# Performance work log

Hardware: AMD Instinct MI355X
Metric: run time of the kernel (lower is better)

The kernel has to match this reference:

```python
import jax, jax.numpy as jnp
import numpy as np

B, GRID, C, K = 8, 24, 768, 3          # batch, ViT patch grid, embed dim, PatchMaker patchsize
PRE_DIM, TGT_DIM = 1024, 1024          # pretrain_embed_dimension, target_embed_dimension
N_MEM, IMG = 20000, 384                # coreset memory bank size, input image size


def adaptive_avg_pool_matrix(lin, lout):
    """Dense matrix M (lout, lin) so that x @ M.T == F.adaptive_avg_pool1d(x, lout)."""
    M = np.zeros((lout, lin), dtype=np.float32)
    for i in range(lout):
        s = (i * lin) // lout
        e = -(((-(i + 1)) * lin) // lout)  # ceil((i+1)*lin/lout)
        M[i, s:e] = 1.0 / (e - s)
    return jnp.asarray(M)


def unfold3x3(x):
    """torch.nn.Unfold(kernel=3, stride=1, pad=1): (B,C,H,W) -> (B, H*W, C, 3, 3)."""
    b, c, h, w = x.shape
    xp = jnp.pad(x, ((0, 0), (0, 0), (1, 1), (1, 1)))
    # stack shifted views in torch Unfold's (C, kh, kw) channel-major order
    p = jnp.stack([xp[:, :, i:i + h, j:j + w] for i in range(K) for j in range(K)], axis=2)
    p = p.reshape(b, c, K, K, h * w).transpose(0, 4, 1, 2, 3)
    return p


def setup_inputs() -> dict:
    key = jax.random.key(0)
    k1, k2, k3, k4 = jax.random.split(key, 4)
    return {
        "feats6": jax.random.normal(k1, (B, GRID * GRID + 1, C), jnp.float32),
        "feats8": jax.random.normal(k2, (B, GRID * GRID + 1, C), jnp.float32),
        "feats10": jax.random.normal(k3, (B, GRID * GRID + 1, C), jnp.float32),
        "memory_bank": jax.random.normal(k4, (N_MEM, TGT_DIM), jnp.float32),
    }


def reference(feats6, feats8, feats10, memory_bank):
    Mpre = adaptive_avg_pool_matrix(C * K * K, PRE_DIM)   # MeanMapper pooling
    Magg = adaptive_avg_pool_matrix(3 * PRE_DIM, TGT_DIM)  # Aggregator pooling

    pooled = []
    for f in (feats6, feats8, feats10):
        # drop CLS token, reshape to CNN-like grid (B, C, 24, 24)
        g = f[:, 1:, :].reshape(B, GRID, GRID, C).transpose(0, 3, 1, 2)
        # patchify (all layers share the 24x24 grid, so the bilinear re-alignment
        # to ref_num_patches in the original code is an identity here)
        p = unfold3x3(g).reshape(B * GRID * GRID, C * K * K)
        pooled.append(p @ Mpre.T)                         # (N, PRE_DIM)
    feats = jnp.stack(pooled, axis=1).reshape(-1, 3 * PRE_DIM)
    emb = feats @ Magg.T                                  # (N, TGT_DIM)

    # squared-L2 nearest neighbour against coreset memory bank (FaissNN IndexFlatL2)
    d2 = (jnp.sum(emb * emb, axis=1, keepdims=True)
          + jnp.sum(memory_bank * memory_bank, axis=1)[None, :]
          - 2.0 * emb @ memory_bank.T)                    # (N, N_MEM)
    patch_scores = jnp.min(d2, axis=1)                    # anomaly_score_num_nn = 1

    ps = patch_scores.reshape(B, GRID, GRID)
    image_scores = jnp.max(ps.reshape(B, -1), axis=1)     # PatchMaker.score (max over patches)
    masks = jax.image.resize(ps, (B, IMG, IMG), method="bilinear")  # RescaleSegmentor
    return image_scores, masks
```

## Files before the change

### kernel.cpp

```cpp
#include <hip/hip_runtime.h>
#include <hip/hip_bf16.h>
#include <stdint.h>

#define B_      8
#define GRID_   24
#define C_      768
#define NPATCH  (B_*GRID_*GRID_)
#define PRE     1024
#define TGT     1024
#define NMEM    20000
#define NMEM_PAD 20096
#define IMG_    384
#define SEQ     577

typedef __bf16 bf16_t;
typedef bf16_t bf16x8 __attribute__((ext_vector_type(8)));
typedef bf16_t bf16x4 __attribute__((ext_vector_type(4)));
typedef float  floatx4 __attribute__((ext_vector_type(4)));

__global__ __launch_bounds__(256) void emb_kernel(
    const float* __restrict__ f6, const float* __restrict__ f8,
    const float* __restrict__ f10,
    bf16_t* __restrict__ emb, float* __restrict__ enorm)
{
    __shared__ float pooled[3*PRE];
    __shared__ float red[4];

    const int n   = blockIdx.x;
    const int b   = n / (GRID_*GRID_);
    const int yx  = n - b*(GRID_*GRID_);
    const int y   = yx / GRID_;
    const int x   = yx - y*GRID_;
    const int t   = threadIdx.x;

    const float* fl[3] = {f6, f8, f10};

#pragma unroll
    for (int l = 0; l < 3; ++l) {
        const float* f = fl[l];
        float A0 = 0.f, B0 = 0.f, C1 = 0.f, D1 = 0.f, E2 = 0.f, F2 = 0.f;
#pragma unroll
        for (int k = 0; k < 9; ++k) {
            const int kh = k / 3, kw = k - kh*3;
            const int ny = y + kh - 1, nx = x + kw - 1;
            const bool v = (ny >= 0 && ny < GRID_ && nx >= 0 && nx < GRID_);
            const int off = v ? (b*SEQ + 1 + ny*GRID_ + nx) : (b*SEQ);
            const float* p = f + (size_t)off*C_ + 3*t;
            float a = p[0], bq = p[1], c = p[2];
            if (!v) { a = 0.f; bq = 0.f; c = 0.f; }
            if (k <= 6) A0 += a;
            if (k >= 6) B0 += a;
            if (k <= 4) C1 += bq;
            if (k >= 4) D1 += bq;
            if (k <= 2) E2 += c;
            if (k >= 2) F2 += c;
        }
        float4 pv;
        pv.x = A0 * (1.f/7.f);
        pv.y = (B0 + C1) * (1.f/8.f);
        pv.z = (D1 + E2) * (1.f/8.f);
        pv.w = F2 * (1.f/7.f);
        *(float4*)(pooled + l*PRE + 4*t) = pv;
    }
    __syncthreads();

    float psq = 0.f;
    bf16x4 ev;
#pragma unroll
    for (int r = 0; r < 4; ++r) {
        const int j = 4*t + r;
        float vv = (pooled[3*j] + pooled[3*j+1] + pooled[3*j+2]) * (1.f/3.f);
        ev[r] = (bf16_t)vv;
        psq += vv*vv;
    }
    *(bf16x4*)(emb + (size_t)n*TGT + 4*t) = ev;

    for (int off = 32; off > 0; off >>= 1) psq += __shfl_down(psq, off, 64);
    if ((t & 63) == 0) red[t >> 6] = psq;
    __syncthreads();
    if (t == 0) enorm[n] = (red[0] + red[1]) + (red[2] + red[3]);
}

__global__ __launch_bounds__(256) void mprep_kernel(
    const float* __restrict__ mb, bf16_t* __restrict__ mbf,
    float* __restrict__ mnorm)
{
    const int r = blockIdx.x;
    const int t = threadIdx.x;
    __shared__ float red[4];
    float psq = 0.f;
    if (r < NMEM) {
        float4 v = ((const float4*)(mb + (size_t)r*TGT))[t];
        bf16x4 o;
        o[0] = (bf16_t)v.x; o[1] = (bf16_t)v.y;
        o[2] = (bf16_t)v.z; o[3] = (bf16_t)v.w;
        ((bf16x4*)(mbf + (size_t)r*TGT))[t] = o;
        psq = v.x*v.x + v.y*v.y + v.z*v.z + v.w*v.w;
    } else {
        bf16x4 z; z[0] = z[1] = z[2] = z[3] = (bf16_t)0.f;
        ((bf16x4*)(mbf + (size_t)r*TGT))[t] = z;
    }
    for (int off = 32; off > 0; off >>= 1) psq += __shfl_down(psq, off, 64);
    if ((t & 63) == 0) red[t >> 6] = psq;
    __syncthreads();
    if (t == 0) mnorm[r] = (r < NMEM) ? ((red[0]+red[1])+(red[2]+red[3])) : 1e30f;
}

__global__ void init_kernel(int* __restrict__ p)
{
    int i = blockIdx.x*256 + threadIdx.x;
    if (i < NPATCH) p[i] = 0x7f7f7f7f;
}

__device__ __forceinline__ void load_lds16(const void* g, void* l)
{
    __builtin_amdgcn_global_load_lds(
        (__attribute__((address_space(1))) void*)g,
        (__attribute__((address_space(3))) void*)l, 16, 0, 0);
}

__global__ __launch_bounds__(256) void nnmin_kernel(
    const bf16_t* __restrict__ E, const bf16_t* __restrict__ M,
    const float* __restrict__ enorm, const float* __restrict__ mnorm,
    int* __restrict__ out_min)
{
    __shared__ __attribute__((aligned(16))) bf16_t As[128*32];
    __shared__ __attribute__((aligned(16))) bf16_t Bs[128*32];

    const int m0   = blockIdx.x * 128;
    const int n0   = blockIdx.y * 128;
    const int tid  = threadIdx.x;
    const int wave = tid >> 6;
    const int lane = tid & 63;
    const int wm   = wave >> 1;
    const int wn   = wave & 1;

    const int sr   = lane >> 2;
    const int slot = lane & 3;
    const int kg   = slot ^ ((sr >> 1) & 3);

    const bf16_t* gA0 = E + (size_t)(m0 + wave*16 + sr)*TGT + kg*8;
    const bf16_t* gA1 = gA0 + (size_t)64*TGT;
    const bf16_t* gB0 = M + (size_t)(n0 + wave*16 + sr)*TGT + kg*8;
    const bf16_t* gB1 = gB0 + (size_t)64*TGT;
    bf16_t* lA0 = As + wave*512 + lane*8;
    bf16_t* lA1 = lA0 + 64*32;
    bf16_t* lB0 = Bs + wave*512 + lane*8;
    bf16_t* lB1 = lB0 + 64*32;

    floatx4 acc[4][4];
#pragma unroll
    for (int i = 0; i < 4; ++i)
#pragma unroll
        for (int j = 0; j < 4; ++j) acc[i][j] = (floatx4)0.0f;

    const int fr = lane & 15;
    const int fg = lane >> 4;
    const int sg = fg ^ ((fr >> 1) & 3);

    for (int k0 = 0; k0 < TGT; k0 += 32) {
        load_lds16(gA0 + k0, lA0);
        load_lds16(gA1 + k0, lA1);
        load_lds16(gB0 + k0, lB0);
        load_lds16(gB1 + k0, lB1);
        __syncthreads();

        bf16x8 a[4], b[4];
#pragma unroll
        for (int t = 0; t < 4; ++t)
            a[t] = *(const bf16x8*)(As + (wm*64 + t*16 + fr)*32 + sg*8);
#pragma unroll
        for (int t = 0; t < 4; ++t)
            b[t] = *(const bf16x8*)(Bs + (wn*64 + t*16 + fr)*32 + sg*8);
#pragma unroll
        for (int tm = 0; tm < 4; ++tm)
#pragma unroll
            for (int tn = 0; tn < 4; ++tn)
                acc[tm][tn] = __builtin_amdgcn_mfma_f32_16x16x32_bf16(
                    a[tm], b[tn], acc[tm][tn], 0, 0, 0);
        __syncthreads();
    }

    const int col  = lane & 15;
    const int rowq = (lane >> 4) * 4;
    const int colbase = n0 + wn*64;
#pragma unroll
    for (int tm = 0; tm < 4; ++tm) {
#pragma unroll
        for (int r = 0; r < 4; ++r) {
            int row = m0 + wm*64 + tm*16 + rowq + r;
            float en = enorm[row];
            float best = 1e38f;
#pragma unroll
            for (int tn = 0; tn < 4; ++tn) {
                float d2 = en + mnorm[colbase + tn*16 + col]
                         - 2.0f * acc[tm][tn][r];
                best = fminf(best, d2);
            }
#pragma unroll
            for (int off = 1; off < 16; off <<= 1)
                best = fminf(best, __shfl_xor(best, off, 64));
            if (col == 0)
                atomicMin(&out_min[row], __float_as_int(best));
        }
    }
}

__global__ __launch_bounds__(256) void score_kernel(
    const int* __restrict__ ps_bits, float* __restrict__ out)
{
    const int b = blockIdx.x, tid = threadIdx.x;
    __shared__ float red[4];
    float m = -1e38f;
    for (int i = tid; i < GRID_*GRID_; i += 256)
        m = fmaxf(m, __int_as_float(ps_bits[b*GRID_*GRID_ + i]));
    for (int off = 32; off > 0; off >>= 1) m = fmaxf(m, __shfl_down(m, off, 64));
    if ((tid & 63) == 0) red[tid >> 6] = m;
    __syncthreads();
    if (tid == 0) out[b] = fmaxf(fmaxf(red[0], red[1]), fmaxf(red[2], red[3]));
}

__global__ __launch_bounds__(256) void mask_kernel(
    const int* __restrict__ ps_bits, float* __restrict__ masks)
{
    int idx = blockIdx.x*256 + threadIdx.x;
    int b  = idx / (IMG_*IMG_);
    int p  = idx - b*(IMG_*IMG_);
    int oy = p / IMG_, ox = p - oy*IMG_;

    float fy = (oy + 0.5f) * (1.0f/16.0f) - 0.5f;
    float fx = (ox + 0.5f) * (1.0f/16.0f) - 0.5f;
    int y0 = (int)floorf(fy); float ty = fy - (float)y0;
    int x0 = (int)floorf(fx); float tx = fx - (float)x0;
    int y0c = min(max(y0, 0), GRID_-1), y1c = min(max(y0+1, 0), GRID_-1);
    int x0c = min(max(x0, 0), GRID_-1), x1c = min(max(x0+1, 0), GRID_-1);

    const int* psb = ps_bits + b*GRID_*GRID_;
    float v00 = __int_as_float(psb[y0c*GRID_ + x0c]);
    float v01 = __int_as_float(psb[y0c*GRID_ + x1c]);
    float v10 = __int_as_float(psb[y1c*GRID_ + x0c]);
    float v11 = __int_as_float(psb[y1c*GRID_ + x1c]);
    float v0 = v00 + (v01 - v00)*tx;
    float v1 = v10 + (v11 - v10)*tx;
    masks[idx] = v0 + (v1 - v0)*ty;
}

extern "C" void kernel_launch(void* const* d_in, const int* in_sizes, int n_in,
                              void* d_out, int out_size, void* d_ws, size_t ws_size,
                              hipStream_t stream)
{
    const float* f6  = (const float*)d_in[0];
    const float* f8  = (const float*)d_in[1];
    const float* f10 = (const float*)d_in[2];
    const float* mb  = (const float*)d_in[3];
    float* out = (float*)d_out;

    char* ws = (char*)d_ws;
    bf16_t* emb  = (bf16_t*)ws;  ws += (size_t)NPATCH*TGT*sizeof(bf16_t);
    bf16_t* mbf  = (bf16_t*)ws;  ws += (size_t)NMEM_PAD*TGT*sizeof(bf16_t);
    float* enorm = (float*)ws;   ws += (size_t)NPATCH*sizeof(float);
    float* mnorm = (float*)ws;   ws += (size_t)NMEM_PAD*sizeof(float);
    int* psbits  = (int*)ws;     ws += (size_t)NPATCH*sizeof(int);

    hipLaunchKernelGGL(emb_kernel, dim3(NPATCH), dim3(256), 0, stream,
                       f6, f8, f10, emb, enorm);
    hipLaunchKernelGGL(mprep_kernel, dim3(NMEM_PAD), dim3(256), 0, stream,
                       mb, mbf, mnorm);
    hipLaunchKernelGGL(init_kernel, dim3((NPATCH+255)/256), dim3(256), 0, stream,
                       psbits);
    hipLaunchKernelGGL(nnmin_kernel, dim3(NPATCH/128, NMEM_PAD/128), dim3(256),
                       0, stream, emb, mbf, enorm, mnorm, psbits);
    hipLaunchKernelGGL(score_kernel, dim3(B_), dim3(256), 0, stream,
                       psbits, out);
    hipLaunchKernelGGL(mask_kernel, dim3((B_*IMG_*IMG_)/256), dim3(256), 0, stream,
                       psbits, out + B_);
}
```

Baseline: 435.0 us.

## Use 256x256 tiles with 4-stage LDS pipeline and register double-buffering in NN GEMM

Rewrites the nearest-neighbour GEMM kernel to use 256x256 output tiles with 512 threads, a 4-deep ring of LDS buffers filled by async global-to-LDS loads, and ping-pong A fragment registers, so loads overlap MFMA work with one barrier per k-step. Memory bank padding grows to a multiple of 256 to match the larger tile. MFMA sections raise wave priority. This aims to cut global traffic per FLOP and hide load latency, at the cost of more registers, 128KB of LDS per block, and more padded rows.

```diff
diff --git a/kernel.cpp b/kernel.cpp
--- a/kernel.cpp
+++ b/kernel.cpp
@@ -9,7 +9,7 @@
 #define PRE     1024
 #define TGT     1024
 #define NMEM    20000
-#define NMEM_PAD 20096
+#define NMEM_PAD 20224
 #define IMG_    384
 #define SEQ     577
 
@@ -119,88 +119,130 @@
         (__attribute__((address_space(3))) void*)l, 16, 0, 0);
 }
 
-__global__ __launch_bounds__(256) void nnmin_kernel(
+#define SYNC_V(N) do { \
+    asm volatile("s_waitcnt vmcnt(" #N ") lgkmcnt(0)" ::: "memory"); \
+    __builtin_amdgcn_s_barrier(); } while (0)
+
+__global__ __launch_bounds__(512, 2) void nnmin_kernel(
     const bf16_t* __restrict__ E, const bf16_t* __restrict__ M,
     const float* __restrict__ enorm, const float* __restrict__ mnorm,
     int* __restrict__ out_min)
 {
-    __shared__ __attribute__((aligned(16))) bf16_t As[128*32];
-    __shared__ __attribute__((aligned(16))) bf16_t Bs[128*32];
-
-    const int m0   = blockIdx.x * 128;
-    const int n0   = blockIdx.y * 128;
+    __shared__ __attribute__((aligned(16))) bf16_t SA[4][256*32];
+    __shared__ __attribute__((aligned(16))) bf16_t SB[4][256*32];
+
+    const int m0   = blockIdx.x * 256;
+    const int n0   = blockIdx.y * 256;
     const int tid  = threadIdx.x;
+    const int lane = tid & 63;
     const int wave = tid >> 6;
-    const int lane = tid & 63;
-    const int wm   = wave >> 1;
-    const int wn   = wave & 1;
-
-    const int sr   = lane >> 2;
-    const int slot = lane & 3;
-    const int kg   = slot ^ ((sr >> 1) & 3);
-
-    const bf16_t* gA0 = E + (size_t)(m0 + wave*16 + sr)*TGT + kg*8;
-    const bf16_t* gA1 = gA0 + (size_t)64*TGT;
-    const bf16_t* gB0 = M + (size_t)(n0 + wave*16 + sr)*TGT + kg*8;
-    const bf16_t* gB1 = gB0 + (size_t)64*TGT;
-    bf16_t* lA0 = As + wave*512 + lane*8;
-    bf16_t* lA1 = lA0 + 64*32;
-    bf16_t* lB0 = Bs + wave*512 + lane*8;
-    bf16_t* lB1 = lB0 + 64*32;
-
-    floatx4 acc[4][4];
-#pragma unroll
-    for (int i = 0; i < 4; ++i)
-#pragma unroll
-        for (int j = 0; j < 4; ++j) acc[i][j] = (floatx4)0.0f;
+    const int wm   = wave >> 2;
+    const int wn   = wave & 3;
+
+    const int srow = tid >> 2;
+    const int slot = tid & 3;
+    const int kg   = slot ^ ((srow >> 1) & 3);
+
+    const bf16_t* gA0 = E + (size_t)(m0 + srow)*TGT + kg*8;
+    const bf16_t* gA1 = gA0 + (size_t)128*TGT;
+    const bf16_t* gB0 = M + (size_t)(n0 + srow)*TGT + kg*8;
+    const bf16_t* gB1 = gB0 + (size_t)128*TGT;
+    const int lofs = tid * 8;
 
     const int fr = lane & 15;
     const int fg = lane >> 4;
-    const int sg = fg ^ ((fr >> 1) & 3);
-
-    for (int k0 = 0; k0 < TGT; k0 += 32) {
-        load_lds16(gA0 + k0, lA0);
-        load_lds16(gA1 + k0, lA1);
-        load_lds16(gB0 + k0, lB0);
-        load_lds16(gB1 + k0, lB1);
-        __syncthreads();
-
-        bf16x8 a[4], b[4];
-#pragma unroll
-        for (int t = 0; t < 4; ++t)
-            a[t] = *(const bf16x8*)(As + (wm*64 + t*16 + fr)*32 + sg*8);
-#pragma unroll
-        for (int t = 0; t < 4; ++t)
-            b[t] = *(const bf16x8*)(Bs + (wn*64 + t*16 + fr)*32 + sg*8);
-#pragma unroll
-        for (int tm = 0; tm < 4; ++tm)
+    int aoff[8], boff[4];
+#pragma unroll
+    for (int tm = 0; tm < 8; ++tm) {
+        const int row = wm*128 + tm*16 + fr;
+        aoff[tm] = row*32 + (fg ^ ((row >> 1) & 3))*8;
+    }
+#pragma unroll
+    for (int tn = 0; tn < 4; ++tn) {
+        const int row = wn*64 + tn*16 + fr;
+        boff[tn] = row*32 + (fg ^ ((row >> 1) & 3))*8;
+    }
+
+    floatx4 acc[8][4];
+#pragma unroll
+    for (int i = 0; i < 8; ++i)
+#pragma unroll
+        for (int j = 0; j < 4; ++j) acc[i][j] = (floatx4)0.0f;
+
+#define STAGE(t) do { \
+    bf16_t* _a = &SA[(t)&3][lofs]; \
+    bf16_t* _b = &SB[(t)&3][lofs]; \
+    const int _ko = (t)*32; \
+    load_lds16(gA0 + _ko, _a); \
+    load_lds16(gA1 + _ko, _a + 4096); \
+    load_lds16(gB0 + _ko, _b); \
+    load_lds16(gB1 + _ko, _b + 4096); } while (0)
+
+#define READ_A(t, A_) do { const bf16_t* _p = SA[(t)&3]; \
+    _Pragma("unroll") \
+    for (int _m = 0; _m < 8; ++_m) A_[_m] = *(const bf16x8*)(_p + aoff[_m]); } while (0)
+
+#define READ_B(t, B_) do { const bf16_t* _p = SB[(t)&3]; \
+    _Pragma("unroll") \
+    for (int _n = 0; _n < 4; ++_n) B_[_n] = *(const bf16x8*)(_p + boff[_n]); } while (0)
+
+#define MFMA_ALL(A_, B_) do { \
+    __builtin_amdgcn_s_setprio(1); \
+    _Pragma("unroll") \
+    for (int _m = 0; _m < 8; ++_m) \
+    _Pragma("unroll") \
+    for (int _n = 0; _n < 4; ++_n) \
+        acc[_m][_n] = __builtin_amdgcn_mfma_f32_16x16x32_bf16(A_[_m], B_[_n], acc[_m][_n], 0, 0, 0); \
+    __builtin_amdgcn_s_setprio(0); } while (0)
+
+    bf16x8 aE[8], aO[8], bb[4];
+
+    STAGE(0); STAGE(1); STAGE(2);
+    asm volatile("s_waitcnt vmcnt(4)" ::: "memory");
+    __builtin_amdgcn_s_barrier();
+    READ_A(0, aE);
+
+    for (int t = 0; t < 28; t += 2) {
+        STAGE(t+3);
+        READ_B(t,   bb);
+        READ_A(t+1, aO);
+        MFMA_ALL(aE, bb);
+        SYNC_V(4);
+        STAGE(t+4);
+        READ_B(t+1, bb);
+        READ_A(t+2, aE);
+        MFMA_ALL(aO, bb);
+        SYNC_V(4);
+    }
+    STAGE(31); READ_B(28, bb); READ_A(29, aO); MFMA_ALL(aE, bb); SYNC_V(4);
+               READ_B(29, bb); READ_A(30, aE); MFMA_ALL(aO, bb); SYNC_V(0);
+               READ_B(30, bb); READ_A(31, aO); MFMA_ALL(aE, bb);
+               READ_B(31, bb);                 MFMA_ALL(aO, bb);
+
+#undef STAGE
+#undef READ_A
+#undef READ_B
+#undef MFMA_ALL
+
+    float mn[4];
+#pragma unroll
+    for (int tn = 0; tn < 4; ++tn)
+        mn[tn] = mnorm[n0 + wn*64 + tn*16 + fr];
+    const int rowq = fg * 4;
+#pragma unroll
+    for (int tm = 0; tm < 8; ++tm) {
+#pragma unroll
+        for (int r = 0; r < 4; ++r) {
+            const int row = m0 + wm*128 + tm*16 + rowq + r;
+            const float en = enorm[row];
+            float best = 1e38f;
 #pragma unroll
             for (int tn = 0; tn < 4; ++tn)
-                acc[tm][tn] = __builtin_amdgcn_mfma_f32_16x16x32_bf16(
-                    a[tm], b[tn], acc[tm][tn], 0, 0, 0);
-        __syncthreads();
-    }
-
-    const int col  = lane & 15;
-    const int rowq = (lane >> 4) * 4;
-    const int colbase = n0 + wn*64;
-#pragma unroll
-    for (int tm = 0; tm < 4; ++tm) {
-#pragma unroll
-        for (int r = 0; r < 4; ++r) {
-            int row = m0 + wm*64 + tm*16 + rowq + r;
-            float en = enorm[row];
-            float best = 1e38f;
-#pragma unroll
-            for (int tn = 0; tn < 4; ++tn) {
-                float d2 = en + mnorm[colbase + tn*16 + col]
-                         - 2.0f * acc[tm][tn][r];
-                best = fminf(best, d2);
-            }
+                best = fminf(best, en + mn[tn] - 2.0f*acc[tm][tn][r]);
 #pragma unroll
             for (int off = 1; off < 16; off <<= 1)
                 best = fminf(best, __shfl_xor(best, off, 64));
-            if (col == 0)
+            if (fr == 0)
                 atomicMin(&out_min[row], __float_as_int(best));
         }
     }
@@ -268,7 +310,7 @@
                        mb, mbf, mnorm);
     hipLaunchKernelGGL(init_kernel, dim3((NPATCH+255)/256), dim3(256), 0, stream,
                        psbits);
-    hipLaunchKernelGGL(nnmin_kernel, dim3(NPATCH/128, NMEM_PAD/128), dim3(256),
+    hipLaunchKernelGGL(nnmin_kernel, dim3(NPATCH/256, NMEM_PAD/256), dim3(512),
                        0, stream, emb, mbf, enorm, mnorm, psbits);
     hipLaunchKernelGGL(score_kernel, dim3(B_), dim3(256), 0, stream,
                        psbits, out);
```

Result: slower. 470.1 us (+8.1%).
